# Kernel tuning notes

Measured on AMD Instinct MI355X. Metric: run time of the kernel, lower is better.

## Reference

```python
import jax, jax.numpy as jnp
import numpy as np

K = 20
BN_EPS = 1e-5


def setup_inputs() -> dict:
    key = jax.random.key(0)
    ks = jax.random.split(key, 8)
    B, N, C = 4, 8192, 128
    x = jax.random.normal(ks[0], (B, C, N), dtype=jnp.float32)
    xyz = jax.random.normal(ks[1], (B, N, 3), dtype=jnp.float32)
    # Conv1d(C+3 -> C, kernel_size=1): weight [C, C+3], bias [C]
    w1 = jax.random.normal(ks[2], (C, C + 3), dtype=jnp.float32) * 0.05
    b1 = jax.random.normal(ks[3], (C,), dtype=jnp.float32) * 0.05
    gamma = jnp.ones((C,), dtype=jnp.float32)
    beta = jnp.zeros((C,), dtype=jnp.float32)
    # Conv1d(C -> C, kernel_size=1)
    w2 = jax.random.normal(ks[4], (C, C), dtype=jnp.float32) * 0.05
    b2 = jax.random.normal(ks[5], (C,), dtype=jnp.float32) * 0.05
    return {"x": x, "xyz": xyz, "w1": w1, "b1": b1, "gamma": gamma,
            "beta": beta, "w2": w2, "b2": b2}


def _compute_normals(xyz):
    # xyz: [B, N, 3]
    sq = jnp.sum(xyz * xyz, axis=-1)                      # [B, N]
    dist = (-2.0 * jnp.einsum('bnc,bmc->bnm', xyz, xyz)
            + sq[:, :, None] + sq[:, None, :])            # [B, N, N]
    _, idx = jax.lax.top_k(-dist, K)                      # smallest-k -> [B, N, k]
    neighbors = jax.vmap(lambda pts, ix: pts[ix])(xyz, idx)  # [B, N, k, 3]
    nb = neighbors - xyz[:, :, None, :]                   # centered
    cov = jnp.einsum('bnkc,bnkd->bncd', nb, nb)           # [B, N, 3, 3]
    _, eigvecs = jnp.linalg.eigh(cov)                     # ascending eigenvalues
    return eigvecs[..., :, 0]                             # normal = smallest-eig vector, [B, N, 3]


def reference(x, xyz, w1, b1, gamma, beta, w2, b2):
    normals = _compute_normals(xyz)                       # [B, N, 3]
    geo = jnp.concatenate([x, jnp.transpose(normals, (0, 2, 1))], axis=1)  # [B, C+3, N]
    h = jnp.einsum('oc,bcn->bon', w1, geo) + b1[None, :, None]
    # BatchNorm1d (training mode, biased variance over (B, N))
    mean = jnp.mean(h, axis=(0, 2), keepdims=True)
    var = jnp.mean((h - mean) ** 2, axis=(0, 2), keepdims=True)
    h = gamma[None, :, None] * (h - mean) * jax.lax.rsqrt(var + BN_EPS) + beta[None, :, None]
    h = jax.nn.relu(h)
    out = jnp.einsum('oc,bcn->bon', w2, h) + b2[None, :, None]
    return out
```

## Files before the change

### kernel.cpp

```cpp
#include <hip/hip_runtime.h>
#include <math.h>

#define N_PTS 8192
#define BATCH 4
#define CH 128
#define KNN 20
#define CAP 91
#define STQ 93
#define POOL 256


__device__ __forceinline__ float slapy2f(float x, float y) {
#pragma clang fp contract(off)
  float ax = fabsf(x), ay = fabsf(y);
  float w = fmaxf(ax, ay), z = fminf(ax, ay);
  if (z == 0.0f) return w;
  float t = z / w;
  return w * sqrtf(1.0f + t * t);
}

__device__ __forceinline__ void slartgf(float f, float g, float* cs, float* sn, float* r) {
#pragma clang fp contract(off)
  if (g == 0.0f) { *cs = 1.0f; *sn = 0.0f; *r = f; }
  else if (f == 0.0f) { *cs = 0.0f; *sn = copysignf(1.0f, g); *r = fabsf(g); }
  else {
    float f1 = fabsf(f);
    float d = sqrtf(f * f + g * g);
    *cs = f1 / d;
    *r = copysignf(d, f);
    *sn = g / (*r);
  }
}

__device__ void slaev2f(float a, float b, float c, float* rt1, float* rt2,
                        float* cs1, float* sn1) {
#pragma clang fp contract(off)
  float sm = a + c, df = a - c, adf = fabsf(df);
  float tb = b + b, ab = fabsf(tb);
  float acmx, acmn;
  if (fabsf(a) > fabsf(c)) { acmx = a; acmn = c; } else { acmx = c; acmn = a; }
  float rt;
  if (adf > ab)      { float q = ab / adf;  rt = adf * sqrtf(1.0f + q * q); }
  else if (adf < ab) { float q = adf / ab;  rt = ab * sqrtf(1.0f + q * q); }
  else               rt = ab * sqrtf(2.0f);
  int sgn1;
  if (sm < 0.0f)      { *rt1 = 0.5f * (sm - rt); sgn1 = -1; *rt2 = (acmx / *rt1) * acmn - (b / *rt1) * b; }
  else if (sm > 0.0f) { *rt1 = 0.5f * (sm + rt); sgn1 = 1;  *rt2 = (acmx / *rt1) * acmn - (b / *rt1) * b; }
  else                { *rt1 = 0.5f * rt; *rt2 = -0.5f * rt; sgn1 = 1; }
  float cs; int sgn2;
  if (df >= 0.0f) { cs = df + rt; sgn2 = 1; } else { cs = df - rt; sgn2 = -1; }
  float acs = fabsf(cs);
  if (acs > ab) {
    float ct = -tb / cs;
    *sn1 = 1.0f / sqrtf(1.0f + ct * ct);
    *cs1 = ct * (*sn1);
  } else {
    if (ab == 0.0f) { *cs1 = 1.0f; *sn1 = 0.0f; }
    else {
      float tn = -cs / tb;
      *cs1 = 1.0f / sqrtf(1.0f + tn * tn);
      *sn1 = tn * (*cs1);
    }
  }
  if (sgn1 == sgn2) { float tn = *cs1; *cs1 = -(*sn1); *sn1 = tn; }
}

__device__ void eigh3_smallest(float a00, float a10, float a20,
                               float a11, float a21, float a22, float evec[3]) {
#pragma clang fp contract(off)
  float d[3], e[2], tau = 0.0f, v2 = 0.0f;
  d[0] = a00;
  {
    float xnorm = sqrtf(a20 * a20);
    if (xnorm == 0.0f) {
      tau = 0.0f; v2 = 0.0f;
      e[0] = a10; d[1] = a11; e[1] = a21; d[2] = a22;
    } else {
      float alpha = a10;
      float beta = -copysignf(slapy2f(alpha, xnorm), alpha);
      tau = (beta - alpha) / beta;
      float invs = 1.0f / (alpha - beta);
      v2 = a20 * invs;
      e[0] = beta;
      float y0 = tau * a11;
      float y1 = tau * a21;
      y0 = y0 + tau * (a21 * v2);
      y1 = y1 + (tau * v2) * a22;
      float dot = y0 + y1 * v2;
      float al = (-0.5f * tau) * dot;
      float w0 = y0 + al;
      float w1 = y1 + al * v2;
      a11 = (a11 - w0) - w0;
      a21 = (a21 - v2 * w0) - w1;
      a22 = (a22 - v2 * w1) - w1 * v2;
      d[1] = a11; e[1] = a21; d[2] = a22;
    }
  }

  float z[3][3] = {{1.0f,0.0f,0.0f},{0.0f,1.0f,0.0f},{0.0f,0.0f,1.0f}};
  const float eps = 5.9604644775390625e-08f;
  const float eps2 = 3.5527136788005009e-15f;
  const float safmin = 1.1754943508222875e-38f;
  int nmaxit = 90, jtot = 0;
  int l1 = 0;
  int l, m, lend, lsv, lendsv;
  float p, g, r, c, s, f, b_, rt1, rt2, tst;
  float wc[2], wsn[2];

outer_loop:
  if (l1 > 2) goto sorting;
  if (l1 > 0) e[l1 - 1] = 0.0f;
  {
    int mm;
    for (mm = l1; mm <= 1; ++mm) {
      tst = fabsf(e[mm]);
      if (tst == 0.0f) break;
      if (tst <= (sqrtf(fabsf(d[mm])) * sqrtf(fabsf(d[mm + 1]))) * eps) { e[mm] = 0.0f; break; }
    }
    m = (mm > 1) ? 2 : mm;
  }
  l = l1; lsv = l; lend = m; lendsv = lend; l1 = m + 1;
  if (lend == l) goto outer_loop;
  {
    float an = 0.0f;
    for (int i2 = l; i2 <= lend; ++i2) an = fmaxf(an, fabsf(d[i2]));
    for (int i2 = l; i2 < lend; ++i2) an = fmaxf(an, fabsf(e[i2]));
    if (an == 0.0f) goto outer_loop;
  }
  if (fabsf(d[lend]) < fabsf(d[l])) { lend = lsv; l = lendsv; }

  if (lend > l) {
ql40:
    if (l != lend) {
      for (m = l; m <= lend - 1; ++m) {
        tst = e[m] * e[m];
        if (tst <= (eps2 * fabsf(d[m])) * fabsf(d[m + 1]) + safmin) goto ql60;
      }
    }
    m = lend;
ql60:
    if (m < lend) e[m] = 0.0f;
    p = d[l];
    if (m == l) goto ql80;
    if (m == l + 1) {
      slaev2f(d[l], e[l], d[l + 1], &rt1, &rt2, &c, &s);
      for (int i2 = 0; i2 < 3; ++i2) {
        float temp = z[i2][l + 1];
        z[i2][l + 1] = c * temp - s * z[i2][l];
        z[i2][l]     = s * temp + c * z[i2][l];
      }
      d[l] = rt1; d[l + 1] = rt2; e[l] = 0.0f;
      l += 2;
      if (l <= lend) goto ql40;
      goto done140;
    }
    if (jtot == nmaxit) goto done140;
    jtot++;
    g = (d[l + 1] - p) / (2.0f * e[l]);
    r = slapy2f(g, 1.0f);
    g = d[m] - p + e[l] / (g + copysignf(r, g));
    s = 1.0f; c = 1.0f; p = 0.0f;
    for (int i2 = m - 1; i2 >= l; --i2) {
      f = s * e[i2]; b_ = c * e[i2];
      slartgf(g, f, &c, &s, &r);
      if (i2 != m - 1) e[i2 + 1] = r;
      g = d[i2 + 1] - p;
      r = (d[i2] - g) * s + 2.0f * c * b_;
      p = s * r;
      d[i2 + 1] = g + p;
      g = c * r - b_;
      wc[i2] = c; wsn[i2] = -s;
    }
    for (int j = m - 1; j >= l; --j) {
      float ct = wc[j], st = wsn[j];
      for (int i2 = 0; i2 < 3; ++i2) {
        float temp = z[i2][j + 1];
        z[i2][j + 1] = ct * temp - st * z[i2][j];
        z[i2][j]     = st * temp + ct * z[i2][j];
      }
    }
    d[l] -= p;
    e[l] = g;
    goto ql40;
ql80:
    d[l] = p;
    l += 1;
    if (l <= lend) goto ql40;
    goto done140;
  } else {
qr90:
    if (l != lend) {
      for (m = l; m >= lend + 1; --m) {
        tst = e[m - 1] * e[m - 1];
        if (tst <= (eps2 * fabsf(d[m])) * fabsf(d[m - 1]) + safmin) goto qr110;
      }
    }
    m = lend;
qr110:
    if (m > lend) e[m - 1] = 0.0f;
    p = d[l];
    if (m == l) goto qr130;
    if (m == l - 1) {
      slaev2f(d[l - 1], e[l - 1], d[l], &rt1, &rt2, &c, &s);
      for (int i2 = 0; i2 < 3; ++i2) {
        float temp = z[i2][l];
        z[i2][l]     = c * temp - s * z[i2][l - 1];
        z[i2][l - 1] = s * temp + c * z[i2][l - 1];
      }
      d[l - 1] = rt1; d[l] = rt2; e[l - 1] = 0.0f;
      l -= 2;
      if (l >= lend) goto qr90;
      goto done140;
    }
    if (jtot == nmaxit) goto done140;
    jtot++;
    g = (d[l - 1] - p) / (2.0f * e[l - 1]);
    r = slapy2f(g, 1.0f);
    g = d[m] - p + e[l - 1] / (g + copysignf(r, g));
    s = 1.0f; c = 1.0f; p = 0.0f;
    for (int i2 = m; i2 <= l - 1; ++i2) {
      f = s * e[i2]; b_ = c * e[i2];
      slartgf(g, f, &c, &s, &r);
      if (i2 != m) e[i2 - 1] = r;
      g = d[i2] - p;
      r = (d[i2 + 1] - g) * s + 2.0f * c * b_;
      p = s * r;
      d[i2] = g + p;
      g = c * r - b_;
      wc[i2] = c; wsn[i2] = s;
    }
    for (int j = m; j <= l - 1; ++j) {
      float ct = wc[j], st = wsn[j];
      for (int i2 = 0; i2 < 3; ++i2) {
        float temp = z[i2][j + 1];
        z[i2][j + 1] = ct * temp - st * z[i2][j];
        z[i2][j]     = st * temp + ct * z[i2][j];
      }
    }
    d[l] -= p;
    e[l - 1] = g;
    goto qr90;
qr130:
    d[l] = p;
    l -= 1;
    if (l >= lend) goto qr90;
    goto done140;
  }
done140:
  if (jtot < nmaxit) goto outer_loop;
sorting:
  for (int ii = 1; ii <= 2; ++ii) {
    int i_ = ii - 1, k = i_;
    p = d[i_];
    for (int j = ii; j <= 2; ++j) if (d[j] < p) { k = j; p = d[j]; }
    if (k != i_) {
      d[k] = d[i_]; d[i_] = p;
      for (int i2 = 0; i2 < 3; ++i2) { float tz = z[i2][i_]; z[i2][i_] = z[i2][k]; z[i2][k] = tz; }
    }
  }
  {
    float z10 = z[1][0], z20 = z[2][0];
    float sum = z10 + v2 * z20;
    evec[0] = z[0][0];
    evec[1] = z10 - tau * sum;
    evec[2] = z20 - tau * sum * v2;
  }
}

__global__ __launch_bounds__(256) void prep_kernel(const float* __restrict__ xyz,
                                                   const float* __restrict__ w1,
                                                   const float* __restrict__ w2,
                                                   float4* __restrict__ xyz4,
                                                   float* __restrict__ w1t,
                                                   float* __restrict__ w2t,
                                                   float* __restrict__ stats) {
  int idx = blockIdx.x * 256 + threadIdx.x;
  if (idx < BATCH * N_PTS) {
    float x = xyz[idx * 3], y = xyz[idx * 3 + 1], zz = xyz[idx * 3 + 2];
    float sq = fmaf(zz, zz, fmaf(y, y, x * x));
    xyz4[idx] = make_float4(x, y, zz, -0.5f * sq);
  }
  if (idx < 132 * CH) {
    int cc = idx >> 7, o = idx & 127;
    w1t[idx] = (cc < 131) ? w1[o * 131 + cc] : 0.0f;
  }
  if (idx < CH * CH) {
    int cc = idx >> 7, o = idx & 127;
    w2t[idx] = w2[o * CH + cc];
  }
  if (idx < 256) stats[idx] = 0.0f;
}

__device__ __forceinline__ float qdist2(const float4 qv, const float4 cv) {
  float dot = fmaf(qv.x, cv.x, fmaf(qv.y, cv.y, qv.z * cv.z));
  return fmaf(-2.0f, dot, (-2.0f * qv.w) + (-2.0f * cv.w));
}

__device__ __forceinline__ unsigned int distbits(float dist) {
  unsigned int du = __float_as_uint(dist);
  return (du & 0x80000000u) ? ~du : (du | 0x80000000u);
}

__global__ __launch_bounds__(512) void knn_select_kernel(const float4* __restrict__ xyz4,
                                                         unsigned short* __restrict__ nidx) {
  __shared__ unsigned long long pool[POOL];
  __shared__ unsigned int lst_d[64 * STQ];
  __shared__ unsigned short lst_i[64 * STQ];
  __shared__ float bnd[8 * 64];
  __shared__ unsigned int qcnt[64];
  __shared__ unsigned int qflag[64];
  __shared__ unsigned int qover[64];
  __shared__ unsigned int pool_cnt;

  const int t = threadIdx.x;
  const int w = t >> 6, l = t & 63;
  const int batch = blockIdx.x >> 7;
  const int q0 = (blockIdx.x & 127) << 6;
  const float4* __restrict__ xb = xyz4 + batch * N_PTS;
  const float4 qv = xb[q0 + l];
  const float qw = -2.0f * qv.w;

  if (t < 64) { qcnt[t] = 0; qflag[t] = 0; qover[t] = 0; }
  if (t == 0) pool_cnt = 0;
  __syncthreads();

  const int base = __builtin_amdgcn_readfirstlane(w * 1024);

  float a0 = -INFINITY, a1 = -INFINITY, a2 = -INFINITY;
  float b0 = -INFINITY, b1 = -INFINITY, b2 = -INFINITY;
#pragma unroll 4
  for (int i = 0; i < 1024; i += 2) {
    float4 cva = xb[base + i];
    float4 cvb = xb[base + i + 1];
    float ka = fmaf(qv.x, cva.x, fmaf(qv.y, cva.y, fmaf(qv.z, cva.z, cva.w)));
    float kb = fmaf(qv.x, cvb.x, fmaf(qv.y, cvb.y, fmaf(qv.z, cvb.z, cvb.w)));
    float ta0 = fminf(a0, ka); a0 = fmaxf(a0, ka);
    float tb0 = fminf(b0, kb); b0 = fmaxf(b0, kb);
    float ta1 = fminf(a1, ta0); a1 = fmaxf(a1, ta0);
    float tb1 = fminf(b1, tb0); b1 = fmaxf(b1, tb0);
    a2 = fmaxf(a2, ta1);
    b2 = fmaxf(b2, tb1);
  }
  {
    float t0, t1;
    t0 = fminf(a0, b0); a0 = fmaxf(a0, b0); t1 = fminf(a1, t0); a1 = fmaxf(a1, t0); a2 = fmaxf(a2, t1);
    t0 = fminf(a0, b1); a0 = fmaxf(a0, b1); t1 = fminf(a1, t0); a1 = fmaxf(a1, t0); a2 = fmaxf(a2, t1);
    t0 = fminf(a0, b2); a0 = fmaxf(a0, b2); t1 = fminf(a1, t0); a1 = fmaxf(a1, t0); a2 = fmaxf(a2, t1);
  }
  bnd[w * 64 + l] = a2;
  __syncthreads();

  float kmin = bnd[l];
#pragma unroll
  for (int ww = 1; ww < 8; ++ww) kmin = fminf(kmin, bnd[ww * 64 + l]);
  float Tq = fmaf(-2.0f, kmin, qw);
  Tq = Tq + (fabsf(Tq) * 2e-5f + 1e-3f);
  const float thK = 0.5f * (qw - Tq) - 1e-3f;

#pragma unroll 4
  for (int i = 0; i < 1024; ++i) {
    float4 cv = xb[base + i];
    float k = fmaf(qv.x, cv.x, fmaf(qv.y, cv.y, fmaf(qv.z, cv.z, cv.w)));
    if (k >= thK) {
      float dot = fmaf(qv.x, cv.x, fmaf(qv.y, cv.y, qv.z * cv.z));
      float dist = fmaf(-2.0f, dot, qw + (-2.0f * cv.w));
      if (dist <= Tq) {
        unsigned int db = distbits(dist);
        unsigned int pos = atomicAdd(&qcnt[l], 1u);
        if (pos < CAP) {
          lst_d[l * STQ + pos] = db;
          lst_i[l * STQ + pos] = (unsigned short)(base + i);
        } else {
          unsigned long long key = ((unsigned long long)db << 32)
                                 | ((unsigned int)l << 16) | (unsigned int)(base + i);
          unsigned int pp = atomicAdd(&pool_cnt, 1u);
          if (pp < POOL) { pool[pp] = key; qflag[l] = 1u; }
          else qover[l] = 1u;
        }
      }
    }
  }
  __syncthreads();

  const int qg = t >> 3, sub = t & 7;
  unsigned int n = qcnt[qg]; if (n > CAP) n = CAP;
  const unsigned int pcnt = (qflag[qg] && !qover[qg]) ? min(pool_cnt, (unsigned int)POOL) : 0u;
  unsigned short* oq = nidx + ((size_t)(batch * N_PTS + q0 + qg)) * KNN;

  if (qover[qg]) {
    if (sub == 0) {
      unsigned long long best[KNN];
#pragma unroll
      for (int j = 0; j < KNN; ++j) best[j] = ~0ULL;
      const float4 qv2 = xb[q0 + qg];
      for (int m = 0; m < N_PTS; ++m) {
        float dist = qdist2(qv2, xb[m]);
        unsigned long long p = ((unsigned long long)distbits(dist) << 32) | (unsigned int)m;
        if (p < best[KNN - 1]) {
          int j = KNN - 1;
          while (j > 0 && best[j - 1] > p) { best[j] = best[j - 1]; --j; }
          best[j] = p;
        }
      }
      for (int j = 0; j < KNN; ++j) oq[j] = (unsigned short)(best[j] & 0xffffu);
    }
  } else {
    for (int r = 0; r < KNN; ++r) {
      unsigned long long best = ~0ULL; int bslot = 0;
      for (unsigned int s = sub; s < n; s += 8) {
        unsigned long long v = ((unsigned long long)lst_d[qg * STQ + s] << 16)
                             | (unsigned long long)lst_i[qg * STQ + s];
        if (v < best) { best = v; bslot = (int)s; }
      }
      for (unsigned int s = sub; s < pcnt; s += 8) {
        unsigned long long v = pool[s];
        if ((unsigned int)((v >> 16) & 0xffffu) == (unsigned int)qg) {
          unsigned long long pv = ((v >> 32) << 16) | (v & 0xffffULL);
          if (pv < best) { best = pv; bslot = 0x10000 | (int)s; }
        }
      }
#pragma unroll
      for (int mm = 1; mm < 8; mm <<= 1) {
        unsigned long long ob = __shfl_xor(best, mm, 64);
        int obs = __shfl_xor(bslot, mm, 64);
        if (ob < best) { best = ob; bslot = obs; }
      }
      int s = bslot & 0xffff;
      if ((s & 7) == sub) {
        if (bslot & 0x10000) pool[s] = ~0ULL;
        else lst_d[qg * STQ + s] = 0xFFFFFFFFu;
      }
      if (sub == 0) oq[r] = (unsigned short)(best & 0xffffu);
    }
  }
}

__global__ __launch_bounds__(256) void normals_kernel(const float4* __restrict__ xyz4,
                                                      const unsigned short* __restrict__ nidx,
                                                      float4* __restrict__ nrm4) {
  int gid = blockIdx.x * 256 + threadIdx.x;
  int batch = gid >> 13, q = gid & (N_PTS - 1);
  const float4* __restrict__ xb = xyz4 + batch * N_PTS;
  const float4 qv = xb[q];
  const unsigned short* iq = nidx + (size_t)gid * KNN;
  float c00, c01, c02, c11, c12, c22;
  {
#pragma clang fp contract(off)
    c00 = 0.f; c01 = 0.f; c02 = 0.f; c11 = 0.f; c12 = 0.f; c22 = 0.f;
    for (int j = 0; j < KNN; ++j) {
      float4 pv = xb[iq[j]];
      float dx = pv.x - qv.x, dy = pv.y - qv.y, dz = pv.z - qv.z;
      c00 = c00 + dx * dx; c01 = c01 + dx * dy; c02 = c02 + dx * dz;
      c11 = c11 + dy * dy; c12 = c12 + dy * dz; c22 = c22 + dz * dz;
    }
  }
  float ev[3];
  eigh3_smallest(c00, c01, c02, c11, c12, c22, ev);
  nrm4[gid] = make_float4(ev[0], ev[1], ev[2], 0.0f);
}

__global__ __launch_bounds__(256) void gemm1_stats_kernel(const float* __restrict__ x,
                                                          const float4* __restrict__ nrm4,
                                                          const float* __restrict__ w1t,
                                                          const float* __restrict__ b1,
                                                          float* __restrict__ sums,
                                                          float* __restrict__ sumsq) {
  __shared__ float lds[64 * 134];
  const int t = threadIdx.x;
  const int b = blockIdx.x >> 7;
  const int n0 = (blockIdx.x & 127) << 6;
  for (int idx = t; idx < CH * 64; idx += 256) {
    int cc = idx >> 6, nl = idx & 63;
    lds[nl * 134 + cc] = x[((size_t)(b * CH + cc)) * N_PTS + n0 + nl];
  }
  if (t < 64) {
    float4 nv = nrm4[b * N_PTS + n0 + t];
    lds[t * 134 + 128] = nv.x; lds[t * 134 + 129] = nv.y;
    lds[t * 134 + 130] = nv.z; lds[t * 134 + 131] = 0.0f;
  }
  __syncthreads();

  const int og = __builtin_amdgcn_readfirstlane(t >> 6);
  const int nl = t & 63;
  float acc[32];
#pragma unroll
  for (int k = 0; k < 32; ++k) acc[k] = b1[og * 32 + k];
  for (int c2 = 0; c2 < 66; ++c2) {
    float2 xv = *(const float2*)&lds[nl * 134 + 2 * c2];
    const float* wr0 = w1t + (2 * c2) * CH + og * 32;
    const float* wr1 = wr0 + CH;
#pragma unroll
    for (int k = 0; k < 32; ++k) acc[k] = fmaf(wr0[k], xv.x, acc[k]);
#pragma unroll
    for (int k = 0; k < 32; ++k) acc[k] = fmaf(wr1[k], xv.y, acc[k]);
  }
  __syncthreads();
#pragma unroll
  for (int k2 = 0; k2 < 16; ++k2)
    *(float2*)&lds[nl * 134 + og * 32 + 2 * k2] = make_float2(acc[2 * k2], acc[2 * k2 + 1]);
  __syncthreads();
  {
    int cc = t & 127, hf = t >> 7;
    float sm = 0.f, sq = 0.f;
    for (int rr = hf * 32; rr < hf * 32 + 32; ++rr) {
      float v = lds[rr * 134 + cc];
      sm += v; sq = fmaf(v, v, sq);
    }
    atomicAdd(&sums[cc], sm);
    atomicAdd(&sumsq[cc], sq);
  }
}

__global__ void bn_finalize_kernel(const float* __restrict__ sums, const float* __restrict__ sumsq,
                                   const float* __restrict__ gamma, const float* __restrict__ beta,
                                   float* __restrict__ scale, float* __restrict__ shift) {
  int c = threadIdx.x;
  if (c < CH) {
    const double cnt = (double)(BATCH * N_PTS);
    double mean = (double)sums[c] / cnt;
    double var = (double)sumsq[c] / cnt - mean * mean;
    double inv = 1.0 / sqrt(var + 1e-5);
    double sc = (double)gamma[c] * inv;
    scale[c] = (float)sc;
    shift[c] = (float)((double)beta[c] - mean * sc);
  }
}

__global__ __launch_bounds__(256) void fused_out_kernel(const float* __restrict__ x,
                                                        const float4* __restrict__ nrm4,
                                                        const float* __restrict__ w1t,
                                                        const float* __restrict__ b1,
                                                        const float* __restrict__ w2t,
                                                        const float* __restrict__ b2,
                                                        const float* __restrict__ scale,
                                                        const float* __restrict__ shift,
                                                        float* __restrict__ out) {
  __shared__ float lds[64 * 134];
  const int t = threadIdx.x;
  const int b = blockIdx.x >> 7;
  const int n0 = (blockIdx.x & 127) << 6;
  for (int idx = t; idx < CH * 64; idx += 256) {
    int cc = idx >> 6, nl = idx & 63;
    lds[nl * 134 + cc] = x[((size_t)(b * CH + cc)) * N_PTS + n0 + nl];
  }
  if (t < 64) {
    float4 nv = nrm4[b * N_PTS + n0 + t];
    lds[t * 134 + 128] = nv.x; lds[t * 134 + 129] = nv.y;
    lds[t * 134 + 130] = nv.z; lds[t * 134 + 131] = 0.0f;
  }
  __syncthreads();

  const int og = __builtin_amdgcn_readfirstlane(t >> 6);
  const int nl = t & 63;
  float acc[32];
#pragma unroll
  for (int k = 0; k < 32; ++k) acc[k] = b1[og * 32 + k];
  for (int c2 = 0; c2 < 66; ++c2) {
    float2 xv = *(const float2*)&lds[nl * 134 + 2 * c2];
    const float* wr0 = w1t + (2 * c2) * CH + og * 32;
    const float* wr1 = wr0 + CH;
#pragma unroll
    for (int k = 0; k < 32; ++k) acc[k] = fmaf(wr0[k], xv.x, acc[k]);
#pragma unroll
    for (int k = 0; k < 32; ++k) acc[k] = fmaf(wr1[k], xv.y, acc[k]);
  }
#pragma unroll
  for (int k = 0; k < 32; ++k) {
    float sc = scale[og * 32 + k], sh = shift[og * 32 + k];
    acc[k] = fmaxf(fmaf(acc[k], sc, sh), 0.0f);
  }
  __syncthreads();
#pragma unroll
  for (int k2 = 0; k2 < 16; ++k2)
    *(float2*)&lds[nl * 134 + og * 32 + 2 * k2] = make_float2(acc[2 * k2], acc[2 * k2 + 1]);
  __syncthreads();

  float acc2[32];
#pragma unroll
  for (int k = 0; k < 32; ++k) acc2[k] = b2[og * 32 + k];
  for (int c2 = 0; c2 < 64; ++c2) {
    float2 hv = *(const float2*)&lds[nl * 134 + 2 * c2];
    const float* wr0 = w2t + (2 * c2) * CH + og * 32;
    const float* wr1 = wr0 + CH;
#pragma unroll
    for (int k = 0; k < 32; ++k) acc2[k] = fmaf(wr0[k], hv.x, acc2[k]);
#pragma unroll
    for (int k = 0; k < 32; ++k) acc2[k] = fmaf(wr1[k], hv.y, acc2[k]);
  }
#pragma unroll
  for (int k = 0; k < 32; ++k) {
    int o = og * 32 + k;
    out[((size_t)(b * CH + o)) * N_PTS + n0 + nl] = acc2[k];
  }
}

extern "C" void kernel_launch(void* const* d_in, const int* in_sizes, int n_in,
                              void* d_out, int out_size, void* d_ws, size_t ws_size,
                              hipStream_t stream) {
  const float* x     = (const float*)d_in[0];
  const float* xyz   = (const float*)d_in[1];
  const float* w1    = (const float*)d_in[2];
  const float* b1    = (const float*)d_in[3];
  const float* gamma = (const float*)d_in[4];
  const float* beta  = (const float*)d_in[5];
  const float* w2    = (const float*)d_in[6];
  const float* b2    = (const float*)d_in[7];
  float* out = (float*)d_out;

  float* W = (float*)d_ws;
  float4* xyz4 = (float4*)W;
  float4* nrm4 = (float4*)(W + 131072);
  float* w1t   = W + 262144;
  float* w2t   = W + 279040;
  float* stats = W + 295424;
  float* scale = W + 295680;
  float* shift = W + 295808;
  unsigned short* nidx = (unsigned short*)(W + 295936);

  prep_kernel<<<128, 256, 0, stream>>>(xyz, w1, w2, xyz4, w1t, w2t, stats);
  knn_select_kernel<<<BATCH * N_PTS / 64, 512, 0, stream>>>(xyz4, nidx);
  normals_kernel<<<BATCH * N_PTS / 256, 256, 0, stream>>>(xyz4, nidx, nrm4);
  gemm1_stats_kernel<<<BATCH * N_PTS / 64, 256, 0, stream>>>(x, nrm4, w1t, b1, stats, stats + 128);
  bn_finalize_kernel<<<1, 128, 0, stream>>>(stats, stats + 128, gamma, beta, scale, shift);
  fused_out_kernel<<<BATCH * N_PTS / 64, 256, 0, stream>>>(x, nrm4, w1t, b1, w2t, b2, scale, shift, out);
}
```

Baseline: 398.2 us.

## Split KNN candidate scan into 16 chunks over 32 queries per block

The KNN select kernel now handles 32 queries per block instead of 64, and each query's candidate scan is split across 16 chunks of 512 points instead of 8 chunks of 1024. This doubles the block count and halves the serial scan length per thread. Per-query list capacity grows to 176, and the final top-k selection uses 16 lanes per query. The normals kernel also moves to 64-thread blocks so more blocks are launched. In exchange, the per-chunk top-3 bounds are looser, so more candidates pass the threshold and more shared-memory atomics occur. The overflow path may also be hit more often.

```diff
diff --git a/kernel.cpp b/kernel.cpp
--- a/kernel.cpp
+++ b/kernel.cpp
@@ -5,8 +5,10 @@
 #define BATCH 4
 #define CH 128
 #define KNN 20
-#define CAP 91
-#define STQ 93
+#define QPB 32
+#define NCHK 16
+#define CAP 176
+#define STQ 178
 #define POOL 256
 
 
@@ -304,32 +306,34 @@
 __global__ __launch_bounds__(512) void knn_select_kernel(const float4* __restrict__ xyz4,
                                                          unsigned short* __restrict__ nidx) {
   __shared__ unsigned long long pool[POOL];
-  __shared__ unsigned int lst_d[64 * STQ];
-  __shared__ unsigned short lst_i[64 * STQ];
-  __shared__ float bnd[8 * 64];
-  __shared__ unsigned int qcnt[64];
-  __shared__ unsigned int qflag[64];
-  __shared__ unsigned int qover[64];
+  __shared__ unsigned int lst_d[QPB * STQ];
+  __shared__ unsigned short lst_i[QPB * STQ];
+  __shared__ float bnd[NCHK * QPB];
+  __shared__ unsigned int qcnt[QPB];
+  __shared__ unsigned int qflag[QPB];
+  __shared__ unsigned int qover[QPB];
   __shared__ unsigned int pool_cnt;
 
   const int t = threadIdx.x;
   const int w = t >> 6, l = t & 63;
-  const int batch = blockIdx.x >> 7;
-  const int q0 = (blockIdx.x & 127) << 6;
+  const int qi = l & 31;
+  const int chunk = w * 2 + (l >> 5);
+  const int batch = blockIdx.x >> 8;
+  const int q0 = (blockIdx.x & 255) << 5;
   const float4* __restrict__ xb = xyz4 + batch * N_PTS;
-  const float4 qv = xb[q0 + l];
+  const float4 qv = xb[q0 + qi];
   const float qw = -2.0f * qv.w;
 
-  if (t < 64) { qcnt[t] = 0; qflag[t] = 0; qover[t] = 0; }
+  if (t < QPB) { qcnt[t] = 0; qflag[t] = 0; qover[t] = 0; }
   if (t == 0) pool_cnt = 0;
   __syncthreads();
 
-  const int base = __builtin_amdgcn_readfirstlane(w * 1024);
+  const int base = chunk << 9;
 
   float a0 = -INFINITY, a1 = -INFINITY, a2 = -INFINITY;
   float b0 = -INFINITY, b1 = -INFINITY, b2 = -INFINITY;
 #pragma unroll 4
-  for (int i = 0; i < 1024; i += 2) {
+  for (int i = 0; i < 512; i += 2) {
     float4 cva = xb[base + i];
     float4 cvb = xb[base + i + 1];
     float ka = fmaf(qv.x, cva.x, fmaf(qv.y, cva.y, fmaf(qv.z, cva.z, cva.w)));
@@ -347,18 +351,18 @@
     t0 = fminf(a0, b1); a0 = fmaxf(a0, b1); t1 = fminf(a1, t0); a1 = fmaxf(a1, t0); a2 = fmaxf(a2, t1);
     t0 = fminf(a0, b2); a0 = fmaxf(a0, b2); t1 = fminf(a1, t0); a1 = fmaxf(a1, t0); a2 = fmaxf(a2, t1);
   }
-  bnd[w * 64 + l] = a2;
-  __syncthreads();
-
-  float kmin = bnd[l];
-#pragma unroll
-  for (int ww = 1; ww < 8; ++ww) kmin = fminf(kmin, bnd[ww * 64 + l]);
+  bnd[chunk * QPB + qi] = a2;
+  __syncthreads();
+
+  float kmin = bnd[qi];
+#pragma unroll
+  for (int c = 1; c < NCHK; ++c) kmin = fminf(kmin, bnd[c * QPB + qi]);
   float Tq = fmaf(-2.0f, kmin, qw);
   Tq = Tq + (fabsf(Tq) * 2e-5f + 1e-3f);
   const float thK = 0.5f * (qw - Tq) - 1e-3f;
 
 #pragma unroll 4
-  for (int i = 0; i < 1024; ++i) {
+  for (int i = 0; i < 512; ++i) {
     float4 cv = xb[base + i];
     float k = fmaf(qv.x, cv.x, fmaf(qv.y, cv.y, fmaf(qv.z, cv.z, cv.w)));
     if (k >= thK) {
@@ -366,23 +370,23 @@
       float dist = fmaf(-2.0f, dot, qw + (-2.0f * cv.w));
       if (dist <= Tq) {
         unsigned int db = distbits(dist);
-        unsigned int pos = atomicAdd(&qcnt[l], 1u);
+        unsigned int pos = atomicAdd(&qcnt[qi], 1u);
         if (pos < CAP) {
-          lst_d[l * STQ + pos] = db;
-          lst_i[l * STQ + pos] = (unsigned short)(base + i);
+          lst_d[qi * STQ + pos] = db;
+          lst_i[qi * STQ + pos] = (unsigned short)(base + i);
         } else {
           unsigned long long key = ((unsigned long long)db << 32)
-                                 | ((unsigned int)l << 16) | (unsigned int)(base + i);
+                                 | ((unsigned int)qi << 16) | (unsigned int)(base + i);
           unsigned int pp = atomicAdd(&pool_cnt, 1u);
-          if (pp < POOL) { pool[pp] = key; qflag[l] = 1u; }
-          else qover[l] = 1u;
+          if (pp < POOL) { pool[pp] = key; qflag[qi] = 1u; }
+          else qover[qi] = 1u;
         }
       }
     }
   }
   __syncthreads();
 
-  const int qg = t >> 3, sub = t & 7;
+  const int qg = t >> 4, sub = t & 15;
   unsigned int n = qcnt[qg]; if (n > CAP) n = CAP;
   const unsigned int pcnt = (qflag[qg] && !qover[qg]) ? min(pool_cnt, (unsigned int)POOL) : 0u;
   unsigned short* oq = nidx + ((size_t)(batch * N_PTS + q0 + qg)) * KNN;
@@ -407,12 +411,12 @@
   } else {
     for (int r = 0; r < KNN; ++r) {
       unsigned long long best = ~0ULL; int bslot = 0;
-      for (unsigned int s = sub; s < n; s += 8) {
+      for (unsigned int s = sub; s < n; s += 16) {
         unsigned long long v = ((unsigned long long)lst_d[qg * STQ + s] << 16)
                              | (unsigned long long)lst_i[qg * STQ + s];
         if (v < best) { best = v; bslot = (int)s; }
       }
-      for (unsigned int s = sub; s < pcnt; s += 8) {
+      for (unsigned int s = sub; s < pcnt; s += 16) {
         unsigned long long v = pool[s];
         if ((unsigned int)((v >> 16) & 0xffffu) == (unsigned int)qg) {
           unsigned long long pv = ((v >> 32) << 16) | (v & 0xffffULL);
@@ -420,13 +424,13 @@
         }
       }
 #pragma unroll
-      for (int mm = 1; mm < 8; mm <<= 1) {
+      for (int mm = 1; mm < 16; mm <<= 1) {
         unsigned long long ob = __shfl_xor(best, mm, 64);
         int obs = __shfl_xor(bslot, mm, 64);
         if (ob < best) { best = ob; bslot = obs; }
       }
       int s = bslot & 0xffff;
-      if ((s & 7) == sub) {
+      if ((s & 15) == sub) {
         if (bslot & 0x10000) pool[s] = ~0ULL;
         else lst_d[qg * STQ + s] = 0xFFFFFFFFu;
       }
@@ -435,10 +439,10 @@
   }
 }
 
-__global__ __launch_bounds__(256) void normals_kernel(const float4* __restrict__ xyz4,
-                                                      const unsigned short* __restrict__ nidx,
-                                                      float4* __restrict__ nrm4) {
-  int gid = blockIdx.x * 256 + threadIdx.x;
+__global__ __launch_bounds__(64) void normals_kernel(const float4* __restrict__ xyz4,
+                                                     const unsigned short* __restrict__ nidx,
+                                                     float4* __restrict__ nrm4) {
+  int gid = blockIdx.x * 64 + threadIdx.x;
   int batch = gid >> 13, q = gid & (N_PTS - 1);
   const float4* __restrict__ xb = xyz4 + batch * N_PTS;
   const float4 qv = xb[q];
@@ -618,8 +622,8 @@
   unsigned short* nidx = (unsigned short*)(W + 295936);
 
   prep_kernel<<<128, 256, 0, stream>>>(xyz, w1, w2, xyz4, w1t, w2t, stats);
-  knn_select_kernel<<<BATCH * N_PTS / 64, 512, 0, stream>>>(xyz4, nidx);
-  normals_kernel<<<BATCH * N_PTS / 256, 256, 0, stream>>>(xyz4, nidx, nrm4);
+  knn_select_kernel<<<BATCH * N_PTS / QPB, 512, 0, stream>>>(xyz4, nidx);
+  normals_kernel<<<BATCH * N_PTS / 64, 64, 0, stream>>>(xyz4, nidx, nrm4);
   gemm1_stats_kernel<<<BATCH * N_PTS / 64, 256, 0, stream>>>(x, nrm4, w1t, b1, stats, stats + 128);
   bn_finalize_kernel<<<1, 128, 0, stream>>>(stats, stats + 128, gamma, beta, scale, shift);
   fused_out_kernel<<<BATCH * N_PTS / 64, 256, 0, stream>>>(x, nrm4, w1t, b1, w2t, b2, scale, shift, out);
```

New measurement: 481.7 us. 1.21x slower.
